# Optimization experiments

Measured on AMD Instinct MI355X. Metric: run time of the kernel, lower is better.

The kernel has to match this reference:

```python
import jax, jax.numpy as jnp
import numpy as np

BSZ, SEQ, D_IN = 256, 512, 1
STATE, D_OUT, KX = 512, 512, 5


def setup_inputs() -> dict:
    key = jax.random.key(0)
    k1, k2, k3, k4, k5, k6 = jax.random.split(key, 6)
    inputs = jax.random.normal(k1, (BSZ, SEQ, D_IN), dtype=jnp.float32)
    # diagonal transition, kept stable in (0, 0.99)
    A = jax.random.uniform(k2, (STATE,), dtype=jnp.float32, minval=0.0, maxval=0.99)
    B = jax.random.normal(k3, (D_IN, STATE), dtype=jnp.float32) * 0.05
    C = jax.random.normal(k4, (STATE, D_OUT), dtype=jnp.float32) * 0.05
    M = jax.random.normal(k5, (D_OUT, D_IN, KX), dtype=jnp.float32) * 0.05
    h0 = jax.random.normal(k6, (STATE,), dtype=jnp.float32)
    return {"inputs": inputs, "A": A, "B": B, "C": C, "M": M, "h0": h0}


def reference(inputs, A, B, C, M, h0):
    """LDS forward: h_t = A*h_{t-1} + x_t @ B; y_t = h_t @ C + sum_i M[:,:,i] x_{t-1-i}.
    inputs: [B, T, 1] -> out: [B, T, D_OUT]
    """
    bsz, T, _ = inputs.shape
    h_init = jnp.broadcast_to(h0, (bsz, h0.shape[0]))  # reset_state: h = h0 per batch row

    xs = jnp.swapaxes(inputs, 0, 1)  # [T, B, 1]

    def step(h, x_t):
        h = h * A + x_t @ B  # [B, STATE]
        return h, h

    _, hs = jax.lax.scan(step, h_init, xs)  # hs: [T, B, STATE]
    lds_out = jnp.einsum('tbs,so->bto', hs, C)  # [B, T, D_OUT]

    # AR ring buffer: at step t it holds x_{t-1}..x_{t-kx} (zeros before t=0),
    # tap i multiplies M[:,:,i]. With d_in==1 this is a delayed causal conv.
    x = inputs[:, :, 0]  # [B, T]
    kx = M.shape[-1]
    shifted = jnp.stack(
        [jnp.pad(x, ((0, 0), (i + 1, 0)))[:, :T] for i in range(kx)], axis=-1
    )  # [B, T, kx]; entry i is x_{t-1-i}
    ar_out = jnp.einsum('btk,ok->bto', shifted, M[:, 0, :])  # [B, T, D_OUT]

    return lds_out + ar_out
```

## Files before the change

kernel.cpp:

```cpp
#include <hip/hip_runtime.h>


typedef __attribute__((ext_vector_type(8))) short short8v;
typedef __attribute__((ext_vector_type(4))) float float4v;

#define NB 16
#define SIG(e) ((e) + ((e) >> 3))
#define AWI(j) ((((j) % 6) + 6) % 6)

static __device__ __forceinline__ unsigned short f2bf(float f) {
    union { float f; unsigned int u; } x; x.f = f;
    unsigned int r = x.u + 0x7fffu + ((x.u >> 16) & 1u);
    return (unsigned short)(r >> 16);
}

__global__ __launch_bounds__(256) void k_prep(const float* __restrict__ A,
                                              const float* __restrict__ B,
                                              const float* __restrict__ h0,
                                              const float* __restrict__ C,
                                              const float* __restrict__ M,
                                              const float* __restrict__ x,
                                              unsigned short* __restrict__ KT,
                                              float* __restrict__ G,
                                              short8v* __restrict__ XS) {
    __shared__ float PBL[512][4];
    __shared__ float PHL[512][4];
    __shared__ float red[4][64][8];
    __shared__ unsigned short xs[512];
    const int tid = threadIdx.x;

    if (blockIdx.x < 1024) {
        const int d0 = (blockIdx.x & 127) * 4;
        const int oc = blockIdx.x >> 7;

        #pragma unroll
        for (int q = 0; q < 2; ++q) {
            int ss = tid + q * 256;
            float a = A[ss];
            float r = 1.0f, base = a;
            #pragma unroll
            for (int bit = 0; bit < 9; ++bit) {
                if (d0 & (1 << bit)) r *= base;
                base *= base;
            }
            float bs = B[ss], hs = h0[ss];
            #pragma unroll
            for (int j = 0; j < 4; ++j) {
                PBL[ss][j] = r * bs;
                PHL[ss][j] = r * a * hs;
                r *= a;
            }
        }
        __syncthreads();

        const int lane = tid & 63;
        const int sc   = tid >> 6;
        const int o    = oc * 64 + lane;
        float kt[4] = {0.f, 0.f, 0.f, 0.f};
        float gg[4] = {0.f, 0.f, 0.f, 0.f};
        for (int si = 0; si < 128; si += 8) {
            float c8[8];
            #pragma unroll
            for (int u = 0; u < 8; ++u)
                c8[u] = C[(sc * 128 + si + u) * 512 + o];
            #pragma unroll
            for (int u = 0; u < 8; ++u) {
                int s = sc * 128 + si + u;
                #pragma unroll
                for (int j = 0; j < 4; ++j) {
                    kt[j] = fmaf(PBL[s][j], c8[u], kt[j]);
                    gg[j] = fmaf(PHL[s][j], c8[u], gg[j]);
                }
            }
        }
        #pragma unroll
        for (int j = 0; j < 4; ++j) {
            red[sc][lane][j]     = kt[j];
            red[sc][lane][j + 4] = gg[j];
        }
        __syncthreads();
        if (sc == 0) {
            #pragma unroll
            for (int j = 0; j < 4; ++j) {
                float v  = red[0][lane][j] + red[1][lane][j]
                         + red[2][lane][j] + red[3][lane][j];
                float gv = red[0][lane][j+4] + red[1][lane][j+4]
                         + red[2][lane][j+4] + red[3][lane][j+4];
                int d = d0 + j;
                if (d >= 1 && d <= 5) v += M[o * 5 + (d - 1)];
                KT[o * 512 + d] = f2bf(v);
                G[d * 512 + o]  = gv;
            }
        }
    } else {
        const int b = blockIdx.x - 1024;
        #pragma unroll
        for (int q = 0; q < 2; ++q) {
            int i = tid * 2 + q;
            xs[i] = f2bf(x[b * 512 + 511 - i]);
        }
        __syncthreads();
        short8v* dst = XS + (size_t)b * 1216;
        for (int s2 = tid; s2 < 1216; s2 += 256) {
            if (s2 % 9 == 8 || s2 > 1150) dst[s2] = (short8v)(short)0;
        }
        #pragma unroll
        for (int q = 0; q < 4; ++q) {
            int e = tid * 4 + q;
            short8v v;
            #pragma unroll
            for (int jj = 0; jj < 8; ++jj) {
                int i = e + jj;
                v[jj] = (i < 512) ? (short)xs[i] : (short)0;
            }
            dst[SIG(e)] = v;
        }
    }
}

__global__ __launch_bounds__(512, 2) void k_main(const short8v* __restrict__ XS,
                                                 const unsigned short* __restrict__ KT,
                                                 const float* __restrict__ G,
                                                 float* __restrict__ out) {
    __shared__ short8v xbuf[2][1216];

    const int bo0 = blockIdx.x * 32;
    const int b0  = blockIdx.y * NB;
    const int tid = threadIdx.x;
    const int lane = tid & 63;
    const int wv   = tid >> 6;
    const int t0w  = wv * 64;
    const int lrow = lane & 15;
    const int g    = lane >> 4;

    {
        const short8v* src = XS + (size_t)b0 * 1216;
        for (int c = wv; c < 19; c += 8)
            __builtin_amdgcn_global_load_lds(
                (const __attribute__((address_space(1))) void*)(src + c * 64 + lane),
                (__attribute__((address_space(3))) void*)(&xbuf[0][c * 64]),
                16, 0, 0);
    }

    short8v bfr[2][16];
    #pragma unroll
    for (int ni = 0; ni < 2; ++ni) {
        const unsigned short* bp = KT + (bo0 + ni * 16 + lrow) * 512 + g * 8;
        #pragma unroll
        for (int ks = 0; ks < 16; ++ks)
            bfr[ni][ks] = *(const short8v*)(bp + ks * 32);
    }

    float4v gacc[4][2];
    #pragma unroll
    for (int mi = 0; mi < 4; ++mi)
        #pragma unroll
        for (int ni = 0; ni < 2; ++ni)
            gacc[mi][ni] = *(const float4v*)(G + (t0w + mi * 16 + lrow) * 512
                                               + bo0 + ni * 16 + g * 4);

    asm volatile("s_waitcnt vmcnt(0)" ::: "memory");
    __builtin_amdgcn_s_barrier();

    const int E0 = 511 - t0w - lrow + g * 8;

    int p = 0;
    for (int bi = 0; bi < NB; ++bi) {
        const int b = b0 + bi;

        if (bi + 1 < NB) {
            const short8v* src = XS + (size_t)(b + 1) * 1216;
            short8v* dstb = xbuf[p ^ 1];
            for (int c = wv; c < 19; c += 8)
                __builtin_amdgcn_global_load_lds(
                    (const __attribute__((address_space(1))) void*)(src + c * 64 + lane),
                    (__attribute__((address_space(3))) void*)(dstb + c * 64),
                    16, 0, 0);
        }

        const short8v* xo = xbuf[p];

        float4v acc[4][2];
        #pragma unroll
        for (int mi = 0; mi < 4; ++mi)
            #pragma unroll
            for (int ni = 0; ni < 2; ++ni)
                acc[mi][ni] = (float4v)(0.0f);

        short8v aw[6];
        #pragma unroll
        for (int j = -3; j <= 0; ++j)
            aw[AWI(j)] = xo[SIG(E0 + 16 * j)];

        #pragma unroll
        for (int ks = 0; ks < 16; ++ks) {
            acc[3][0] = __builtin_amdgcn_mfma_f32_16x16x32_bf16(
                bfr[0][ks], aw[AWI(2 * ks - 3)], acc[3][0], 0, 0, 0);
            acc[3][1] = __builtin_amdgcn_mfma_f32_16x16x32_bf16(
                bfr[1][ks], aw[AWI(2 * ks - 3)], acc[3][1], 0, 0, 0);
            acc[2][0] = __builtin_amdgcn_mfma_f32_16x16x32_bf16(
                bfr[0][ks], aw[AWI(2 * ks - 2)], acc[2][0], 0, 0, 0);
            acc[2][1] = __builtin_amdgcn_mfma_f32_16x16x32_bf16(
                bfr[1][ks], aw[AWI(2 * ks - 2)], acc[2][1], 0, 0, 0);
            if (ks < 15) {
                aw[AWI(2 * ks + 1)] = xo[SIG(E0 + 16 * (2 * ks + 1))];
                aw[AWI(2 * ks + 2)] = xo[SIG(E0 + 16 * (2 * ks + 2))];
            }
            acc[1][0] = __builtin_amdgcn_mfma_f32_16x16x32_bf16(
                bfr[0][ks], aw[AWI(2 * ks - 1)], acc[1][0], 0, 0, 0);
            acc[1][1] = __builtin_amdgcn_mfma_f32_16x16x32_bf16(
                bfr[1][ks], aw[AWI(2 * ks - 1)], acc[1][1], 0, 0, 0);
            acc[0][0] = __builtin_amdgcn_mfma_f32_16x16x32_bf16(
                bfr[0][ks], aw[AWI(2 * ks)], acc[0][0], 0, 0, 0);
            acc[0][1] = __builtin_amdgcn_mfma_f32_16x16x32_bf16(
                bfr[1][ks], aw[AWI(2 * ks)], acc[0][1], 0, 0, 0);
        }

        float* op = out + (size_t)b * 262144;
        #pragma unroll
        for (int mi = 0; mi < 4; ++mi) {
            const int t = t0w + mi * 16 + lrow;
            float* rp = op + t * 512 + bo0 + g * 4;
            *(float4v*)(rp)      = acc[mi][0] + gacc[mi][0];
            *(float4v*)(rp + 16) = acc[mi][1] + gacc[mi][1];
        }

        if (bi + 1 < NB) {
            asm volatile("s_waitcnt vmcnt(8)" ::: "memory");
            __builtin_amdgcn_s_barrier();
            p ^= 1;
        }
    }
}

extern "C" void kernel_launch(void* const* d_in, const int* in_sizes, int n_in,
                              void* d_out, int out_size, void* d_ws, size_t ws_size,
                              hipStream_t stream) {
    const float* x  = (const float*)d_in[0];
    const float* A  = (const float*)d_in[1];
    const float* B  = (const float*)d_in[2];
    const float* C  = (const float*)d_in[3];
    const float* M  = (const float*)d_in[4];
    const float* h0 = (const float*)d_in[5];
    float* out = (float*)d_out;

    char* ws = (char*)d_ws;
    unsigned short* KT = (unsigned short*)ws;
    float*          G  = (float*)(ws + (1u << 19));
    short8v*        XS = (short8v*)(ws + (1u << 19) + (1u << 20));

    k_prep<<<1280, 256, 0, stream>>>(A, B, h0, C, M, x, KT, G, XS);
    k_main<<<dim3(16, 16), 512, 0, stream>>>(XS, KT, G, out);
}
```

Measured before the change: 91.70 us.

## Retile blocks over time and output, stage results in LDS for coalesced stores

```diff
diff --git a/kernel.cpp b/kernel.cpp
--- a/kernel.cpp
+++ b/kernel.cpp
@@ -123,15 +123,17 @@
                                                  const float* __restrict__ G,
                                                  float* __restrict__ out) {
     __shared__ short8v xbuf[2][1216];
-
-    const int bo0 = blockIdx.x * 32;
-    const int b0  = blockIdx.y * NB;
+    __shared__ float tile[16384];
+
+    const int bo0 = blockIdx.x * 256;
+    const int bt0 = blockIdx.y * 64;
+    const int b0  = blockIdx.z * NB;
     const int tid = threadIdx.x;
     const int lane = tid & 63;
     const int wv   = tid >> 6;
-    const int t0w  = wv * 64;
     const int lrow = lane & 15;
     const int g    = lane >> 4;
+    const int o0w  = bo0 + wv * 32;
 
     {
         const short8v* src = XS + (size_t)b0 * 1216;
@@ -145,7 +147,7 @@
     short8v bfr[2][16];
     #pragma unroll
     for (int ni = 0; ni < 2; ++ni) {
-        const unsigned short* bp = KT + (bo0 + ni * 16 + lrow) * 512 + g * 8;
+        const unsigned short* bp = KT + (o0w + ni * 16 + lrow) * 512 + g * 8;
         #pragma unroll
         for (int ks = 0; ks < 16; ++ks)
             bfr[ni][ks] = *(const short8v*)(bp + ks * 32);
@@ -156,13 +158,14 @@
     for (int mi = 0; mi < 4; ++mi)
         #pragma unroll
         for (int ni = 0; ni < 2; ++ni)
-            gacc[mi][ni] = *(const float4v*)(G + (t0w + mi * 16 + lrow) * 512
-                                               + bo0 + ni * 16 + g * 4);
+            gacc[mi][ni] = *(const float4v*)(G + (bt0 + mi * 16 + lrow) * 512
+                                               + o0w + ni * 16 + g * 4);
 
     asm volatile("s_waitcnt vmcnt(0)" ::: "memory");
     __builtin_amdgcn_s_barrier();
 
-    const int E0 = 511 - t0w - lrow + g * 8;
+    const int E0 = 511 - bt0 - lrow + g * 8;
+    char* tb = (char*)tile;
 
     int p = 0;
     for (int bi = 0; bi < NB; ++bi) {
@@ -216,17 +219,30 @@
                 bfr[1][ks], aw[AWI(2 * ks)], acc[0][1], 0, 0, 0);
         }
 
-        float* op = out + (size_t)b * 262144;
         #pragma unroll
         for (int mi = 0; mi < 4; ++mi) {
-            const int t = t0w + mi * 16 + lrow;
-            float* rp = op + t * 512 + bo0 + g * 4;
-            *(float4v*)(rp)      = acc[mi][0] + gacc[mi][0];
-            *(float4v*)(rp + 16) = acc[mi][1] + gacc[mi][1];
+            const int tl = mi * 16 + lrow;
+            const int sw = (tl & 7) << 4;
+            #pragma unroll
+            for (int ni = 0; ni < 2; ++ni) {
+                const int inrow = wv * 128 + ni * 64 + g * 16;
+                *(float4v*)(tb + tl * 1024 + (inrow ^ sw)) = acc[mi][ni] + gacc[mi][ni];
+            }
+        }
+        asm volatile("s_waitcnt lgkmcnt(0)" ::: "memory");
+        __builtin_amdgcn_s_barrier();
+
+        float* op = out + (size_t)b * 262144 + (size_t)bt0 * 512 + bo0;
+        #pragma unroll
+        for (int rep = 0; rep < 8; ++rep) {
+            const int row = rep * 8 + wv;
+            float4v v = *(const float4v*)(tb + row * 1024
+                                          + ((lane * 16) ^ ((row & 7) << 4)));
+            *(float4v*)(op + row * 512 + lane * 4) = v;
         }
 
         if (bi + 1 < NB) {
-            asm volatile("s_waitcnt vmcnt(8)" ::: "memory");
+            asm volatile("s_waitcnt vmcnt(8) lgkmcnt(0)" ::: "memory");
             __builtin_amdgcn_s_barrier();
             p ^= 1;
         }
@@ -250,5 +266,5 @@
     short8v*        XS = (short8v*)(ws + (1u << 19) + (1u << 20));
 
     k_prep<<<1280, 256, 0, stream>>>(A, B, h0, C, M, x, KT, G, XS);
-    k_main<<<dim3(16, 16), 512, 0, stream>>>(XS, KT, G, out);
-}
+    k_main<<<dim3(2, 8, 16), 512, 0, stream>>>(XS, KT, G, out);
+}
```

Result: slower. 107.3 us (+17.1%).
